# Performance work log

Hardware: AMD Instinct MI355X
Metric: run time of the kernel (lower is better)

## Reference

```python
import jax, jax.numpy as jnp
import numpy as np

B, T, S, L = 1, 2048, 512, 1024
C, H, Hk, D = 2048, 16, 4, 128
THETA = 10000.0


def setup_inputs() -> dict:
    key = jax.random.key(0)
    ks = jax.random.split(key, 9)
    sd = 0.02
    return {
        "x": jax.random.normal(ks[0], (B, T, C), jnp.float32),
        "stm": jax.random.normal(ks[1], (B, S, C), jnp.float32),
        "long_q": jax.random.normal(ks[2], (B, L, H, D), jnp.float32),
        "long_k": jax.random.normal(ks[3], (B, L, Hk, D), jnp.float32),
        "long_v": jax.random.normal(ks[4], (B, L, Hk, D), jnp.float32),
        "Wq": jax.random.normal(ks[5], (C, C), jnp.float32) * sd,
        "Wk": jax.random.normal(ks[6], (C, Hk * D), jnp.float32) * sd,
        "Wv": jax.random.normal(ks[7], (C, Hk * D), jnp.float32) * sd,
        "Wo": jax.random.normal(ks[8], (C, C), jnp.float32) * sd,
    }


def _rope_cos_sin(n, d, theta):
    # precompute_freqs_cis: freqs over even dims, angles t*freq
    freqs = 1.0 / (theta ** (jnp.arange(0, d, 2, dtype=jnp.float32) / d))
    ang = jnp.arange(n, dtype=jnp.float32)[:, None] * freqs[None, :]  # (n, d/2)
    return jnp.cos(ang), jnp.sin(ang)


def _apply_rope(x, cos, sin):
    # x: (B, n, h, D); complex-pair rotation over consecutive dims
    x1, x2 = x[..., 0::2], x[..., 1::2]
    c = cos[None, :, None, :]
    s = sin[None, :, None, :]
    r1 = x1 * c - x2 * s
    r2 = x1 * s + x2 * c
    return jnp.stack([r1, r2], axis=-1).reshape(x.shape)


def reference(x, stm, long_q, long_k, long_v, Wq, Wk, Wv, Wo):
    Bb, Tt, Cc = x.shape
    Ss, Ll = stm.shape[1], long_q.shape[1]
    seq = jnp.concatenate([stm, x], axis=1)  # (B, S+T, C)
    q = jnp.concatenate([long_q, (seq @ Wq).reshape(Bb, Ss + Tt, H, D)], axis=1)
    k = jnp.concatenate([long_k, (seq @ Wk).reshape(Bb, Ss + Tt, Hk, D)], axis=1)
    v = jnp.concatenate([long_v, (seq @ Wv).reshape(Bb, Ss + Tt, Hk, D)], axis=1)
    # inline RoPE on the last T+S positions only (memory bank keeps fixed encoding)
    cos, sin = _rope_cos_sin(Ss + Tt, D, THETA)
    q = q.at[:, Ll:].set(_apply_rope(q[:, Ll:], cos, sin))
    k = k.at[:, Ll:].set(_apply_rope(k[:, Ll:], cos, sin))
    tot = Ll + Ss + Tt
    # structured memory mask: causal over full stream, memory keys (< L+S) visible to all
    idx = jnp.arange(tot)
    mask = (idx[None, :] <= idx[:, None]) | (idx[None, :] < Ll + Ss)  # (tot, tot)
    # GQA: repeat_interleave kv heads
    rep = H // Hk
    kr = jnp.repeat(k, rep, axis=2)  # (B, tot, H, D)
    vr = jnp.repeat(v, rep, axis=2)
    att = jnp.einsum("bihd,bjhd->bhij", q, kr) * (1.0 / np.sqrt(D))
    att = jnp.where(mask[None, None], att, -jnp.inf)
    att = jax.nn.softmax(att, axis=-1)
    y = jnp.einsum("bhij,bjhd->bihd", att, vr).reshape(Bb, tot, Cc)
    y = y[:, -Tt:]  # keep only current-block outputs
    return y @ Wo
```

## Files before the change

kernel.cpp:

```cpp
#include <hip/hip_runtime.h>
#include <hip/hip_bf16.h>

typedef __attribute__((ext_vector_type(8))) short short8;
typedef __attribute__((ext_vector_type(4))) short short4v;
typedef __attribute__((ext_vector_type(4))) float f32x4;
typedef __attribute__((ext_vector_type(4))) float float4v;
typedef __attribute__((ext_vector_type(4))) int i32x4;

#define DEVFN static __device__ __forceinline__

#define T_N   2048
#define S_N   512
#define L_N   1024
#define C_N   2048
#define H_N   16
#define HK_N  4
#define D_N   128
#define ST_N  2560
#define TOT_N 3584
#define KV_N  512

DEVFN short f2bf(float f) {
  union { float f; unsigned u; } v; v.f = f;
  return (short)((v.u + 0x7FFFu + ((v.u >> 16) & 1u)) >> 16);
}
DEVFN float bf2f(short s) {
  union { unsigned u; float f; } v; v.u = ((unsigned)(unsigned short)s) << 16;
  return v.f;
}
DEVFN void gload16(const void* g, void* l) {
  __builtin_amdgcn_global_load_lds(
      (__attribute__((address_space(1))) void*)(g),
      (__attribute__((address_space(3))) void*)(l), 16, 0, 0);
}

#define Q_A (S_N * C_N / 4)
#define Q_B (Q_A + T_N * C_N / 4)
#define Q_C (Q_B + L_N * KV_N / 4)
#define Q_D (Q_C + L_N * KV_N / 4)
#define TAB_E (Q_D + ST_N * 64)
__global__ void k_setup(const float* __restrict__ x, const float* __restrict__ stm,
                        const float* __restrict__ lk, const float* __restrict__ lv,
                        short* __restrict__ seq, short* __restrict__ Kf,
                        short* __restrict__ Vf, float* __restrict__ ct,
                        float* __restrict__ st_) {
  int i = blockIdx.x * 256 + threadIdx.x;
  if (i < Q_D) {
    const float* src; short* dst; int off;
    if (i < Q_A)      { src = stm; dst = seq;                         off = i; }
    else if (i < Q_B) { src = x;   dst = seq + (size_t)S_N * C_N;     off = i - Q_A; }
    else if (i < Q_C) { src = lk;  dst = Kf;                          off = i - Q_B; }
    else              { src = lv;  dst = Vf;                          off = i - Q_C; }
    float4v v = reinterpret_cast<const float4v*>(src)[off];
    short4v o;
    o[0] = f2bf(v[0]); o[1] = f2bf(v[1]); o[2] = f2bf(v[2]); o[3] = f2bf(v[3]);
    reinterpret_cast<short4v*>(dst)[off] = o;
  } else {
    int j = i - Q_D;
    int p = j >> 6, fq = j & 63;
    float freq = expf(-(float)fq * (logf(10000.0f) / 64.0f));
    float ang = (float)p * freq;
    ct[j] = cosf(ang);
    st_[j] = sinf(ang);
  }
}

__global__ void k_tconv_all(const float* __restrict__ Wq, const float* __restrict__ Wk,
                            const float* __restrict__ Wv, const float* __restrict__ Wo,
                            short* __restrict__ WqT, short* __restrict__ WkT,
                            short* __restrict__ WvT, short* __restrict__ WoT) {
  __shared__ float tile[32][33];
  const int z = blockIdx.z;
  const float* in = (z == 0) ? Wq : (z == 1) ? Wk : (z == 2) ? Wv : Wo;
  short* outp     = (z == 0) ? WqT : (z == 1) ? WkT : (z == 2) ? WvT : WoT;
  const int cols = (z == 1 || z == 2) ? KV_N : C_N;
  if (blockIdx.x * 32 >= cols) return;
  int c0 = blockIdx.x * 32, r0 = blockIdx.y * 32;
  int tx = threadIdx.x, ty = threadIdx.y;
#pragma unroll
  for (int i = 0; i < 4; i++)
    tile[ty + i * 8][tx] = in[(size_t)(r0 + ty + i * 8) * cols + c0 + tx];
  __syncthreads();
#pragma unroll
  for (int i = 0; i < 4; i++)
    outp[(size_t)(c0 + ty + i * 8) * C_N + r0 + tx] = f2bf(tile[tx][ty + i * 8]);
}

__global__ void k_tv(const short* __restrict__ vf, short* __restrict__ vt) {
  __shared__ short tile[32][33];
  int hk = blockIdx.z;
  int r0 = blockIdx.x * 32;
  int d0 = blockIdx.y * 32;
  int tx = threadIdx.x, ty = threadIdx.y;
#pragma unroll
  for (int i = 0; i < 4; i++)
    tile[ty + i * 8][tx] = vf[(size_t)(r0 + ty + i * 8) * KV_N + hk * D_N + d0 + tx];
  __syncthreads();
  short* o = vt + (size_t)hk * D_N * TOT_N;
#pragma unroll
  for (int i = 0; i < 4; i++)
    o[(size_t)(d0 + ty + i * 8) * TOT_N + r0 + tx] = tile[tx][ty + i * 8];
}

__global__ __launch_bounds__(256) void k_gemm_o(
    const short* __restrict__ A, const short* __restrict__ Bt,
    float* __restrict__ C) {
  __shared__ short lbuf[2 * 6144];
  const int tid = threadIdx.x;
  const int w = tid >> 6, l = tid & 63;
  const int l15 = l & 15, lh = l >> 4;
  const int f0 = blockIdx.x;
  const int f = ((f0 & 7) << 6) + (f0 >> 3);
  const int rb = (f >> 4) << 6, cb = (f & 15) << 7;
  const int wr = (w >> 1) << 5, wc = (w & 1) << 6;
  f32x4 acc[2][4] = {};
  const int cA = tid;
  const short* pa = &A[(size_t)(rb + (cA >> 2)) * 2048 + (((cA ^ (cA >> 2)) & 3) << 3)];
  const int cB0 = tid, cB1 = 256 + tid;
  const short* pb0 = &Bt[(size_t)(cb + (cB0 >> 2)) * 2048 + (((cB0 ^ (cB0 >> 2)) & 3) << 3)];
  const short* pb1 = &Bt[(size_t)(cb + (cB1 >> 2)) * 2048 + (((cB1 ^ (cB1 >> 2)) & 3) << 3)];
  const int offA  = (w * 64) << 4;
  const int offB0 = 4096 + ((w * 64) << 4);
  const int offB1 = 4096 + ((256 + w * 64) << 4);
  char* lbase = (char*)lbuf;
  const int sw = (lh ^ (l15 & 3)) << 3;
  gload16(pa,  lbase + offA);
  gload16(pb0, lbase + offB0);
  gload16(pb1, lbase + offB1);
  int cur = 0;
  for (int kt = 0; kt < 2048; kt += 32) {
    const bool more = (kt + 32 < 2048);
    if (more) {
      char* p = lbase + (cur ^ 1) * 12288;
      gload16(pa  + kt + 32, p + offA);
      gload16(pb0 + kt + 32, p + offB0);
      gload16(pb1 + kt + 32, p + offB1);
      asm volatile("s_waitcnt vmcnt(3)" ::: "memory");
    } else {
      asm volatile("s_waitcnt vmcnt(0)" ::: "memory");
    }
    __builtin_amdgcn_s_barrier();
    __builtin_amdgcn_sched_barrier(0);
    const short* la = (const short*)(lbase + cur * 12288);
    const short* lb = (const short*)(lbase + cur * 12288 + 4096);
    short8 af[2], bg[4];
#pragma unroll
    for (int m = 0; m < 2; m++)
      af[m] = *reinterpret_cast<const short8*>(&la[(wr + m * 16 + l15) * 32 + sw]);
#pragma unroll
    for (int n = 0; n < 4; n++)
      bg[n] = *reinterpret_cast<const short8*>(&lb[(wc + n * 16 + l15) * 32 + sw]);
    __builtin_amdgcn_s_setprio(1);
#pragma unroll
    for (int m = 0; m < 2; m++)
#pragma unroll
      for (int n = 0; n < 4; n++)
        acc[m][n] = __builtin_amdgcn_mfma_f32_16x16x32_bf16(af[m], bg[n], acc[m][n], 0, 0, 0);
    __builtin_amdgcn_s_setprio(0);
    asm volatile("s_waitcnt lgkmcnt(0)" ::: "memory");
    __builtin_amdgcn_sched_barrier(0);
    __builtin_amdgcn_s_barrier();
    __builtin_amdgcn_sched_barrier(0);
    cur ^= 1;
  }
#pragma unroll
  for (int m = 0; m < 2; m++)
#pragma unroll
    for (int n = 0; n < 4; n++)
#pragma unroll
      for (int r = 0; r < 4; r++) {
        int row = rb + wr + m * 16 + lh * 4 + r;
        int col = cb + wc + n * 16 + l15;
        C[(size_t)row * 2048 + col] = acc[m][n][r];
      }
}

__global__ __launch_bounds__(256) void k_gemm_qkv(
    const short* __restrict__ A, const short* __restrict__ Bt,
    short* __restrict__ qbuf, short* __restrict__ Kf, short* __restrict__ Vf,
    const float* __restrict__ ct, const float* __restrict__ st_) {
  __shared__ short lbuf[2 * 6144];
  const int tid = threadIdx.x;
  const int w = tid >> 6, l = tid & 63;
  const int l15 = l & 15, lh = l >> 4;
  const int f0 = blockIdx.x;
  const int f = (f0 % 8) * 104 + f0 / 8;
  int rb, cb;
  if (f < 512) {
    cb = (f & 15) << 7;
    rb = 512 + ((f >> 4) << 6);
  } else {
    int g = f - 512;
    cb = (16 + (g & 7)) << 7;
    rb = (g >> 3) << 6;
  }
  const int wr = (w >> 1) << 5, wc = (w & 1) << 6;
  f32x4 acc[2][4] = {};
  const int cA = tid;
  const short* pa = &A[(size_t)(rb + (cA >> 2)) * 2048 + (((cA ^ (cA >> 2)) & 3) << 3)];
  const int cB0 = tid, cB1 = 256 + tid;
  const short* pb0 = &Bt[(size_t)(cb + (cB0 >> 2)) * 2048 + (((cB0 ^ (cB0 >> 2)) & 3) << 3)];
  const short* pb1 = &Bt[(size_t)(cb + (cB1 >> 2)) * 2048 + (((cB1 ^ (cB1 >> 2)) & 3) << 3)];
  const int offA  = (w * 64) << 4;
  const int offB0 = 4096 + ((w * 64) << 4);
  const int offB1 = 4096 + ((256 + w * 64) << 4);
  char* lbase = (char*)lbuf;
  const int sw = (lh ^ (l15 & 3)) << 3;
  gload16(pa,  lbase + offA);
  gload16(pb0, lbase + offB0);
  gload16(pb1, lbase + offB1);
  int cur = 0;
  for (int kt = 0; kt < 2048; kt += 32) {
    const bool more = (kt + 32 < 2048);
    if (more) {
      char* p = lbase + (cur ^ 1) * 12288;
      gload16(pa  + kt + 32, p + offA);
      gload16(pb0 + kt + 32, p + offB0);
      gload16(pb1 + kt + 32, p + offB1);
      asm volatile("s_waitcnt vmcnt(3)" ::: "memory");
    } else {
      asm volatile("s_waitcnt vmcnt(0)" ::: "memory");
    }
    __builtin_amdgcn_s_barrier();
    __builtin_amdgcn_sched_barrier(0);
    const short* la = (const short*)(lbase + cur * 12288);
    const short* lb = (const short*)(lbase + cur * 12288 + 4096);
    short8 af[2], bg[4];
#pragma unroll
    for (int m = 0; m < 2; m++)
      af[m] = *reinterpret_cast<const short8*>(&la[(wr + m * 16 + l15) * 32 + sw]);
#pragma unroll
    for (int n = 0; n < 4; n++)
      bg[n] = *reinterpret_cast<const short8*>(&lb[(wc + n * 16 + l15) * 32 + sw]);
    __builtin_amdgcn_s_setprio(1);
#pragma unroll
    for (int m = 0; m < 2; m++)
#pragma unroll
      for (int n = 0; n < 4; n++)
        acc[m][n] = __builtin_amdgcn_mfma_f32_16x16x32_bf16(af[m], bg[n], acc[m][n], 0, 0, 0);
    __builtin_amdgcn_s_setprio(0);
    asm volatile("s_waitcnt lgkmcnt(0)" ::: "memory");
    __builtin_amdgcn_sched_barrier(0);
    __builtin_amdgcn_s_barrier();
    __builtin_amdgcn_sched_barrier(0);
    cur ^= 1;
  }
#pragma unroll
  for (int m = 0; m < 2; m++)
#pragma unroll
    for (int n = 0; n < 4; n++) {
      int coln = cb + wc + n * 16 + l15;
      const bool do_rope = coln < 2560;
      const int fidx = (coln & 127) >> 1;
#pragma unroll
      for (int r = 0; r < 4; r++) {
        int row = rb + wr + m * 16 + lh * 4 + r;
        float v = acc[m][n][r];
        float other = __shfl_xor(v, 1, 64);
        if (do_rope) {
          float co = ct[row * 64 + fidx];
          float si = st_[row * 64 + fidx];
          v = (l15 & 1) ? (other * si + v * co) : (v * co - other * si);
        }
        short bv = f2bf(v);
        if (coln < 2048) {
          if (row >= 512) qbuf[(size_t)(row - 512) * C_N + coln] = bv;
        } else if (coln < 2560) {
          Kf[(size_t)(L_N + row) * KV_N + (coln - 2048)] = bv;
        } else {
          Vf[(size_t)(L_N + row) * KV_N + (coln - 2560)] = bv;
        }
      }
    }
}

__global__ __launch_bounds__(256) void k_attn(
    const short* __restrict__ Q,
    const short* __restrict__ Kf,
    const short* __restrict__ Vt,
    short* __restrict__ Y) {
  __shared__ short kl[2][64 * 128];
  __shared__ short vl[2][128 * 64];
  const int f = blockIdx.x;
  const int hk = f & 3;
  const int qraw = (f >> 2) & 31;
  const int hh = (f >> 7) & 3;
  const int qb = (f & 256) ? (31 - qraw) : qraw;
  const int h = hk * 4 + hh;
  const int tid = threadIdx.x, w = tid >> 6, l = tid & 63;
  const int l15 = l & 15, lh = l >> 4;
  const int qbase = qb << 6;
  const int qrow0 = qbase + (w << 4);
  short8 aq[4];
#pragma unroll
  for (int kb = 0; kb < 4; kb++)
    aq[kb] = *reinterpret_cast<const short8*>(
        &Q[(size_t)(qrow0 + l15) * C_N + h * D_N + kb * 32 + lh * 8]);
  short8 ones;
#pragma unroll
  for (int j = 0; j < 8; j++) ones[j] = (short)0x3F80;
  f32x4 yacc[8] = {};
  f32x4 lacc = {};
  float m_r = -3.0e38f;
  const float K2 = 0.12751744f;
  const float THR = 90.0f;
  const int nkt = (1663 + qbase) >> 6;
  const short* psk[4];
  const short* psv[4];
  int ldsoff[4];
#pragma unroll
  for (int it = 0; it < 4; it++) {
    int c = it * 256 + tid;
    int kr = c >> 4, kkc = c & 15;
    int pkr = (kr & 0x23) | ((kr & 0x0C) << 1) | ((kr >> 2) & 4);
    psk[it] = &Kf[(size_t)pkr * KV_N + hk * D_N + ((kkc ^ (kr & 7)) << 3)];
    int vrow = c >> 3, vkc = c & 7;
    psv[it] = &Vt[(size_t)hk * D_N * TOT_N + (size_t)vrow * TOT_N + ((vkc ^ (vrow & 7)) << 3)];
    ldsoff[it] = (it * 256 + w * 64) << 4;
  }
#pragma unroll
  for (int it = 0; it < 4; it++) gload16(psk[it], (char*)kl + ldsoff[it]);
#pragma unroll
  for (int it = 0; it < 4; it++) gload16(psv[it], (char*)vl + ldsoff[it]);
#pragma unroll
  for (int it = 0; it < 4; it++)
    gload16(psk[it] + 64 * KV_N, (char*)kl + 16384 + ldsoff[it]);
#pragma unroll
  for (int it = 0; it < 4; it++)
    gload16(psv[it] + 64, (char*)vl + 16384 + ldsoff[it]);
  for (int t = 0; t < nkt; t++) {
    if (t + 1 < nkt) asm volatile("s_waitcnt vmcnt(8)" ::: "memory");
    else             asm volatile("s_waitcnt vmcnt(0)" ::: "memory");
    __builtin_amdgcn_s_barrier();
    __builtin_amdgcn_sched_barrier(0);
    const char* kbuf = (const char*)kl + ((t & 1) << 14);
    const char* vbuf = (const char*)vl + ((t & 1) << 14);
    f32x4 s[4] = {};
    __builtin_amdgcn_s_setprio(1);
#pragma unroll
    for (int g = 0; g < 4; g++) {
      int row = g * 16 + l15;
#pragma unroll
      for (int kb = 0; kb < 4; kb++) {
        short8 bk = *reinterpret_cast<const short8*>(
            kbuf + row * 256 + ((((kb << 2) + lh) ^ (row & 7)) << 4));
        s[g] = __builtin_amdgcn_mfma_f32_16x16x32_bf16(bk, aq[kb], s[g], 0, 0, 0);
      }
    }
    __builtin_amdgcn_s_setprio(0);
    if ((t * 64 + 63) > (1536 + qrow0)) {
      int qi = qrow0 + l15;
#pragma unroll
      for (int g = 0; g < 4; g++)
#pragma unroll
        for (int r = 0; r < 4; r++) {
          int key = t * 64 + ((g >> 1) << 5) + (lh << 3) + ((g & 1) << 2) + r;
          if (key > 1536 + qi) s[g][r] = -3.0e38f;
        }
    }
    float lm = s[0][0];
#pragma unroll
    for (int g = 0; g < 4; g++)
#pragma unroll
      for (int r = 0; r < 4; r++) lm = fmaxf(lm, s[g][r]);
    if (!__all(lm <= m_r + THR)) {
      float rm = fmaxf(lm, __shfl_xor(lm, 16, 64));
      rm = fmaxf(rm, __shfl_xor(rm, 32, 64));
      float mn = fmaxf(m_r, rm);
      float scf = __builtin_amdgcn_exp2f((m_r - mn) * K2);
      m_r = mn;
#pragma unroll
      for (int r = 0; r < 4; r++) {
        float sc_c = __shfl(scf, lh * 4 + r, 64);
        lacc[r] *= sc_c;
#pragma unroll
        for (int dg = 0; dg < 8; dg++) yacc[dg][r] *= sc_c;
      }
    }
    const float mk = m_r * K2;
    float pv[16];
#pragma unroll
    for (int g = 0; g < 4; g++)
#pragma unroll
      for (int r = 0; r < 4; r++)
        pv[g * 4 + r] = __builtin_amdgcn_exp2f(s[g][r] * K2 - mk);
    union { i32x4 wv; short8 sv; } u0, u1;
#pragma unroll
    for (int j = 0; j < 4; j++) {
      unsigned w0, w1;
      int g0 = (j >> 1), b0 = g0 * 4 + 2 * (j & 1);
      int g1 = 2 + (j >> 1), b1 = g1 * 4 + 2 * (j & 1);
      asm("v_cvt_pk_bf16_f32 %0, %1, %2" : "=v"(w0) : "v"(pv[b0]), "v"(pv[b0 + 1]));
      asm("v_cvt_pk_bf16_f32 %0, %1, %2" : "=v"(w1) : "v"(pv[b1]), "v"(pv[b1 + 1]));
      u0.wv[j] = (int)w0;
      u1.wv[j] = (int)w1;
    }
    lacc = __builtin_amdgcn_mfma_f32_16x16x32_bf16(u0.sv, ones, lacc, 0, 0, 0);
    lacc = __builtin_amdgcn_mfma_f32_16x16x32_bf16(u1.sv, ones, lacc, 0, 0, 0);
    __builtin_amdgcn_s_setprio(1);
#pragma unroll
    for (int dg = 0; dg < 8; dg++) {
      int vrow = dg * 16 + l15;
      short8 bv0 = *reinterpret_cast<const short8*>(
          vbuf + (vrow << 7) + ((lh ^ (vrow & 7)) << 4));
      yacc[dg] = __builtin_amdgcn_mfma_f32_16x16x32_bf16(u0.sv, bv0, yacc[dg], 0, 0, 0);
      short8 bv1 = *reinterpret_cast<const short8*>(
          vbuf + (vrow << 7) + (((4 + lh) ^ (vrow & 7)) << 4));
      yacc[dg] = __builtin_amdgcn_mfma_f32_16x16x32_bf16(u1.sv, bv1, yacc[dg], 0, 0, 0);
    }
    __builtin_amdgcn_s_setprio(0);
    asm volatile("s_waitcnt lgkmcnt(0)" ::: "memory");
    __builtin_amdgcn_sched_barrier(0);
    __builtin_amdgcn_s_barrier();
    __builtin_amdgcn_sched_barrier(0);
    if (t + 2 < nkt) {
#pragma unroll
      for (int it = 0; it < 4; it++)
        gload16(psk[it] + (size_t)(t + 2) * 64 * KV_N, (char*)kl + ((t & 1) << 14) + ldsoff[it]);
#pragma unroll
      for (int it = 0; it < 4; it++)
        gload16(psv[it] + (size_t)(t + 2) * 64, (char*)vl + ((t & 1) << 14) + ldsoff[it]);
    }
  }
#pragma unroll
  for (int dg = 0; dg < 8; dg++)
#pragma unroll
    for (int r = 0; r < 4; r++) {
      int row = qrow0 + lh * 4 + r;
      int col = h * D_N + dg * 16 + l15;
      Y[(size_t)row * C_N + col] = f2bf(yacc[dg][r] / lacc[r]);
    }
}

extern "C" void kernel_launch(void* const* d_in, const int* in_sizes, int n_in,
                              void* d_out, int out_size, void* d_ws, size_t ws_size,
                              hipStream_t stream) {
  const float* x      = (const float*)d_in[0];
  const float* stm    = (const float*)d_in[1];
  const float* long_k = (const float*)d_in[3];
  const float* long_v = (const float*)d_in[4];
  const float* Wq     = (const float*)d_in[5];
  const float* Wk     = (const float*)d_in[6];
  const float* Wv     = (const float*)d_in[7];
  const float* Wo     = (const float*)d_in[8];
  float* out = (float*)d_out;

  short* seq  = (short*)d_ws;
  short* WqT  = seq  + (size_t)ST_N * C_N;
  short* WkT  = WqT  + (size_t)C_N * C_N;
  short* WvT  = WkT  + (size_t)KV_N * C_N;
  short* WoT  = WvT  + (size_t)KV_N * C_N;
  short* qbuf = WoT  + (size_t)C_N * C_N;
  short* Kf   = qbuf + (size_t)T_N * C_N;
  short* Vf   = Kf   + (size_t)TOT_N * KV_N;
  short* Vt   = Vf   + (size_t)TOT_N * KV_N;
  short* ybuf = Vt   + (size_t)TOT_N * KV_N;
  float* ctab = (float*)(ybuf + (size_t)T_N * C_N);
  float* stab = ctab + (size_t)ST_N * 64;

  k_setup<<<TAB_E / 256, 256, 0, stream>>>(x, stm, long_k, long_v, seq, Kf, Vf, ctab, stab);

  k_tconv_all<<<dim3(64, 64, 4), dim3(32, 8), 0, stream>>>(
      Wq, Wk, Wv, Wo, WqT, WkT, WvT, WoT);

  k_gemm_qkv<<<832, 256, 0, stream>>>(seq, WqT, qbuf, Kf, Vf, ctab, stab);

  k_tv<<<dim3(TOT_N / 32, D_N / 32, HK_N), dim3(32, 8), 0, stream>>>(Vf, Vt);

  k_attn<<<512, 256, 0, stream>>>(qbuf, Kf, Vt, ybuf);

  k_gemm_o<<<512, 256, 0, stream>>>(ybuf, WoT, out);
}
```

Before: 195.8 us.

## Split attention KV range into two partitions with a merge kernel

```diff
diff --git a/kernel.cpp b/kernel.cpp
--- a/kernel.cpp
+++ b/kernel.cpp
@@ -274,18 +274,22 @@
     }
 }
 
-__global__ __launch_bounds__(256) void k_attn(
+__global__ __launch_bounds__(256, 4) void k_attn(
     const short* __restrict__ Q,
     const short* __restrict__ Kf,
     const short* __restrict__ Vt,
-    short* __restrict__ Y) {
-  __shared__ short kl[2][64 * 128];
-  __shared__ short vl[2][128 * 64];
+    short* __restrict__ pY,
+    float* __restrict__ pM,
+    float* __restrict__ pL) {
+  __shared__ short kl[64 * 128];
+  __shared__ short vl[128 * 64];
   const int f = blockIdx.x;
-  const int hk = f & 3;
-  const int qraw = (f >> 2) & 31;
-  const int hh = (f >> 7) & 3;
-  const int qb = (f & 256) ? (31 - qraw) : qraw;
+  const int p = f >> 9;
+  const int f5 = f & 511;
+  const int hk = f5 & 3;
+  const int qraw = (f5 >> 2) & 31;
+  const int hh = (f5 >> 7) & 3;
+  const int qb = (f5 & 256) ? (31 - qraw) : qraw;
   const int h = hk * 4 + hh;
   const int tid = threadIdx.x, w = tid >> 6, l = tid & 63;
   const int l15 = l & 15, lh = l >> 4;
@@ -305,6 +309,9 @@
   const float K2 = 0.12751744f;
   const float THR = 90.0f;
   const int nkt = (1663 + qbase) >> 6;
+  const int th = nkt >> 1;
+  const int t0 = p ? th : 0;
+  const int t1 = p ? nkt : th;
   const short* psk[4];
   const short* psv[4];
   int ldsoff[4];
@@ -319,22 +326,23 @@
     ldsoff[it] = (it * 256 + w * 64) << 4;
   }
 #pragma unroll
-  for (int it = 0; it < 4; it++) gload16(psk[it], (char*)kl + ldsoff[it]);
-#pragma unroll
-  for (int it = 0; it < 4; it++) gload16(psv[it], (char*)vl + ldsoff[it]);
-#pragma unroll
   for (int it = 0; it < 4; it++)
-    gload16(psk[it] + 64 * KV_N, (char*)kl + 16384 + ldsoff[it]);
+    gload16(psk[it] + (size_t)t0 * 64 * KV_N, (char*)kl + ldsoff[it]);
 #pragma unroll
   for (int it = 0; it < 4; it++)
-    gload16(psv[it] + 64, (char*)vl + 16384 + ldsoff[it]);
-  for (int t = 0; t < nkt; t++) {
-    if (t + 1 < nkt) asm volatile("s_waitcnt vmcnt(8)" ::: "memory");
-    else             asm volatile("s_waitcnt vmcnt(0)" ::: "memory");
-    __builtin_amdgcn_s_barrier();
-    __builtin_amdgcn_sched_barrier(0);
-    const char* kbuf = (const char*)kl + ((t & 1) << 14);
-    const char* vbuf = (const char*)vl + ((t & 1) << 14);
+    gload16(psv[it] + (size_t)t0 * 64, (char*)vl + ldsoff[it]);
+  __syncthreads();
+  for (int t = t0; t < t1; t++) {
+    const bool more = (t + 1 < t1);
+    short8 kreg[4], vreg[4];
+    if (more) {
+#pragma unroll
+      for (int it = 0; it < 4; it++)
+        kreg[it] = *reinterpret_cast<const short8*>(psk[it] + (size_t)(t + 1) * 64 * KV_N);
+#pragma unroll
+      for (int it = 0; it < 4; it++)
+        vreg[it] = *reinterpret_cast<const short8*>(psv[it] + (size_t)(t + 1) * 64);
+    }
     f32x4 s[4] = {};
     __builtin_amdgcn_s_setprio(1);
 #pragma unroll
@@ -343,7 +351,7 @@
 #pragma unroll
       for (int kb = 0; kb < 4; kb++) {
         short8 bk = *reinterpret_cast<const short8*>(
-            kbuf + row * 256 + ((((kb << 2) + lh) ^ (row & 7)) << 4));
+            (const char*)kl + row * 256 + ((((kb << 2) + lh) ^ (row & 7)) << 4));
         s[g] = __builtin_amdgcn_mfma_f32_16x16x32_bf16(bk, aq[kb], s[g], 0, 0, 0);
       }
     }
@@ -378,20 +386,20 @@
       }
     }
     const float mk = m_r * K2;
-    float pv[16];
+    float pvv[16];
 #pragma unroll
     for (int g = 0; g < 4; g++)
 #pragma unroll
       for (int r = 0; r < 4; r++)
-        pv[g * 4 + r] = __builtin_amdgcn_exp2f(s[g][r] * K2 - mk);
+        pvv[g * 4 + r] = __builtin_amdgcn_exp2f(s[g][r] * K2 - mk);
     union { i32x4 wv; short8 sv; } u0, u1;
 #pragma unroll
     for (int j = 0; j < 4; j++) {
       unsigned w0, w1;
       int g0 = (j >> 1), b0 = g0 * 4 + 2 * (j & 1);
       int g1 = 2 + (j >> 1), b1 = g1 * 4 + 2 * (j & 1);
-      asm("v_cvt_pk_bf16_f32 %0, %1, %2" : "=v"(w0) : "v"(pv[b0]), "v"(pv[b0 + 1]));
-      asm("v_cvt_pk_bf16_f32 %0, %1, %2" : "=v"(w1) : "v"(pv[b1]), "v"(pv[b1 + 1]));
+      asm("v_cvt_pk_bf16_f32 %0, %1, %2" : "=v"(w0) : "v"(pvv[b0]), "v"(pvv[b0 + 1]));
+      asm("v_cvt_pk_bf16_f32 %0, %1, %2" : "=v"(w1) : "v"(pvv[b1]), "v"(pvv[b1 + 1]));
       u0.wv[j] = (int)w0;
       u1.wv[j] = (int)w1;
     }
@@ -402,10 +410,10 @@
     for (int dg = 0; dg < 8; dg++) {
       int vrow = dg * 16 + l15;
       short8 bv0 = *reinterpret_cast<const short8*>(
-          vbuf + (vrow << 7) + ((lh ^ (vrow & 7)) << 4));
+          (const char*)vl + (vrow << 7) + ((lh ^ (vrow & 7)) << 4));
       yacc[dg] = __builtin_amdgcn_mfma_f32_16x16x32_bf16(u0.sv, bv0, yacc[dg], 0, 0, 0);
       short8 bv1 = *reinterpret_cast<const short8*>(
-          vbuf + (vrow << 7) + (((4 + lh) ^ (vrow & 7)) << 4));
+          (const char*)vl + (vrow << 7) + (((4 + lh) ^ (vrow & 7)) << 4));
       yacc[dg] = __builtin_amdgcn_mfma_f32_16x16x32_bf16(u1.sv, bv1, yacc[dg], 0, 0, 0);
     }
     __builtin_amdgcn_s_setprio(0);
@@ -413,23 +421,51 @@
     __builtin_amdgcn_sched_barrier(0);
     __builtin_amdgcn_s_barrier();
     __builtin_amdgcn_sched_barrier(0);
-    if (t + 2 < nkt) {
+    if (more) {
 #pragma unroll
       for (int it = 0; it < 4; it++)
-        gload16(psk[it] + (size_t)(t + 2) * 64 * KV_N, (char*)kl + ((t & 1) << 14) + ldsoff[it]);
+        *reinterpret_cast<short8*>((char*)kl + ldsoff[it] + (l << 4)) = kreg[it];
 #pragma unroll
       for (int it = 0; it < 4; it++)
-        gload16(psv[it] + (size_t)(t + 2) * 64, (char*)vl + ((t & 1) << 14) + ldsoff[it]);
-    }
+        *reinterpret_cast<short8*>((char*)vl + ldsoff[it] + (l << 4)) = vreg[it];
+    }
+    __syncthreads();
   }
+  const size_t base = (size_t)(p * 16 + h) * 2048;
 #pragma unroll
   for (int dg = 0; dg < 8; dg++)
 #pragma unroll
     for (int r = 0; r < 4; r++) {
       int row = qrow0 + lh * 4 + r;
-      int col = h * D_N + dg * 16 + l15;
-      Y[(size_t)row * C_N + col] = f2bf(yacc[dg][r] / lacc[r]);
-    }
+      pY[(base + row) * 128 + dg * 16 + l15] = f2bf(yacc[dg][r]);
+    }
+#pragma unroll
+  for (int r = 0; r < 4; r++)
+    if (l15 == 0) pL[base + qrow0 + lh * 4 + r] = lacc[r];
+  if (lh == 0) pM[base + qrow0 + l15] = m_r;
+}
+
+__global__ void k_merge(const short* __restrict__ pY, const float* __restrict__ pM,
+                        const float* __restrict__ pL, short* __restrict__ Y) {
+  const int h = blockIdx.y;
+  const int row = blockIdx.x * 16 + (threadIdx.x >> 4);
+  const int d0 = (threadIdx.x & 15) * 8;
+  const size_t b0 = (size_t)h * 2048 + row;
+  const size_t b1 = (size_t)(16 + h) * 2048 + row;
+  const float K2 = 0.12751744f;
+  float m0 = pM[b0], m1 = pM[b1];
+  float l0 = pL[b0], l1 = pL[b1];
+  float M = fmaxf(m0, m1);
+  float a0 = __builtin_amdgcn_exp2f((m0 - M) * K2);
+  float a1 = __builtin_amdgcn_exp2f((m1 - M) * K2);
+  float inv = 1.0f / (l0 * a0 + l1 * a1);
+  short8 y0 = *reinterpret_cast<const short8*>(&pY[b0 * 128 + d0]);
+  short8 y1 = *reinterpret_cast<const short8*>(&pY[b1 * 128 + d0]);
+  short8 o;
+#pragma unroll
+  for (int j = 0; j < 8; j++)
+    o[j] = f2bf((bf2f(y0[j]) * a0 + bf2f(y1[j]) * a1) * inv);
+  *reinterpret_cast<short8*>(&Y[(size_t)row * C_N + h * D_N + d0]) = o;
 }
 
 extern "C" void kernel_launch(void* const* d_in, const int* in_sizes, int n_in,
@@ -458,6 +494,10 @@
   float* ctab = (float*)(ybuf + (size_t)T_N * C_N);
   float* stab = ctab + (size_t)ST_N * 64;
 
+  short* pY = (short*)d_ws;
+  float* pM = (float*)(pY + (size_t)2 * 16 * 2048 * 128);
+  float* pL = pM + (size_t)2 * 16 * 2048;
+
   k_setup<<<TAB_E / 256, 256, 0, stream>>>(x, stm, long_k, long_v, seq, Kf, Vf, ctab, stab);
 
   k_tconv_all<<<dim3(64, 64, 4), dim3(32, 8), 0, stream>>>(
@@ -467,7 +507,9 @@
 
   k_tv<<<dim3(TOT_N / 32, D_N / 32, HK_N), dim3(32, 8), 0, stream>>>(Vf, Vt);
 
-  k_attn<<<512, 256, 0, stream>>>(qbuf, Kf, Vt, ybuf);
+  k_attn<<<1024, 256, 0, stream>>>(qbuf, Kf, Vt, pY, pM, pL);
+
+  k_merge<<<dim3(128, 16), 256, 0, stream>>>(pY, pM, pL, ybuf);
 
   k_gemm_o<<<512, 256, 0, stream>>>(ybuf, WoT, out);
 }
```

After: 200.3 us. +2.3%, slower.
